# Kernel tuning notes

Measured on AMD Instinct MI355X. Metric: run time of the kernel, lower is better.

Reference implementation:

```python
import jax, jax.numpy as jnp
import numpy as np

EPS = 1e-6
NUM_HEADS = 16

def layernorm(x, alpha, bias):
    # Faithful to the torch module: torch.std uses ddof=1, and eps is added to std.
    mean = jnp.mean(x, axis=-1, keepdims=True)
    std = jnp.std(x, axis=-1, keepdims=True, ddof=1)
    return alpha * (x - mean) / (std + EPS) + bias

def setup_inputs() -> dict:
    key = jax.random.key(0)
    B, S, D, F = 4, 2048, 1024, 4096
    ks = jax.random.split(key, 8)
    s = 1.0 / np.sqrt(D)
    inp = {
        'x': jax.random.normal(ks[0], (B, S, D), jnp.float32),
        'src_mask': jnp.ones((B, 1, 1, S), jnp.int32),
        'wq': jax.random.normal(ks[1], (D, D), jnp.float32) * s,
        'bq': jnp.zeros((D,), jnp.float32),
        'wk': jax.random.normal(ks[2], (D, D), jnp.float32) * s,
        'bk': jnp.zeros((D,), jnp.float32),
        'wv': jax.random.normal(ks[3], (D, D), jnp.float32) * s,
        'bv': jnp.zeros((D,), jnp.float32),
        'wo': jax.random.normal(ks[4], (D, D), jnp.float32) * s,
        'bo': jnp.zeros((D,), jnp.float32),
        'w1': jax.random.normal(ks[5], (D, F), jnp.float32) * s,
        'b1': jnp.zeros((F,), jnp.float32),
        'w2': jax.random.normal(ks[6], (F, D), jnp.float32) * (1.0 / np.sqrt(F)),
        'b2': jnp.zeros((D,), jnp.float32),
        'ln1_a': jnp.ones((D,), jnp.float32),
        'ln1_b': jnp.zeros((D,), jnp.float32),
        'ln2_a': jnp.ones((D,), jnp.float32),
        'ln2_b': jnp.zeros((D,), jnp.float32),
    }
    return inp

def mha(x, src_mask, wq, bq, wk, bk, wv, bv, wo, bo):
    B, S, D = x.shape
    H = NUM_HEADS
    dk = D // H
    q = (x @ wq + bq).reshape(B, S, H, dk).transpose(0, 2, 1, 3)  # [B,H,S,dk]
    k = (x @ wk + bk).reshape(B, S, H, dk).transpose(0, 2, 1, 3)
    v = (x @ wv + bv).reshape(B, S, H, dk).transpose(0, 2, 1, 3)
    scores = jnp.einsum('bhqd,bhkd->bhqk', q, k) / np.sqrt(dk)  # [B,H,S,S]
    scores = jnp.where(src_mask == 0, -1e9, scores)
    p = jax.nn.softmax(scores, axis=-1)
    ctx = jnp.einsum('bhqk,bhkd->bhqd', p, v)  # [B,H,S,dk]
    ctx = ctx.transpose(0, 2, 1, 3).reshape(B, S, D)
    return ctx @ wo + bo

def reference(x, src_mask, wq, bq, wk, bk, wv, bv, wo, bo,
              w1, b1, w2, b2, ln1_a, ln1_b, ln2_a, ln2_b):
    # residual 1: pre-norm self-attention (dropout is identity in eval)
    h = x + mha(layernorm(x, ln1_a, ln1_b), src_mask, wq, bq, wk, bk, wv, bv, wo, bo)
    # residual 2: pre-norm FFN
    hn = layernorm(h, ln2_a, ln2_b)
    ffn = jax.nn.relu(hn @ w1 + b1) @ w2 + b2
    return h + ffn
```

## Files before the change

### kernel.cpp

```cpp
#include <hip/hip_runtime.h>
#include <hip/hip_bf16.h>

typedef __attribute__((ext_vector_type(8))) short bf16x8;
typedef __attribute__((ext_vector_type(4))) short bf16x4;
typedef __attribute__((ext_vector_type(4))) float f32x4;
typedef __hip_bfloat16 bf16;
typedef unsigned short u16;

#define B_ 4
#define S_ 2048
#define D_ 1024
#define F_ 4096
#define H_ 16
#define MROWS 8192
#define QSCALE 0.18033688011116012f

__device__ __forceinline__ unsigned pkbf(float lo, float hi){
  union{float f; unsigned u;} a, b; a.f = lo; b.f = hi;
  return __builtin_amdgcn_perm(b.u + 0x8000u, a.u + 0x8000u, 0x07060302);
}
__device__ __forceinline__ u16 bfrnd(float f){
  union{float ff; unsigned u;} c; c.ff = f;
  return (u16)((c.u + 0x8000u) >> 16);
}
__device__ __forceinline__ void gll16(const bf16* gp, u16* lp){
  __builtin_amdgcn_global_load_lds(
      (const __attribute__((address_space(1))) void*)gp,
      (__attribute__((address_space(3))) void*)lp, 16, 0, 0);
}

struct PrepArgs { const float* w[6]; const float* b[3]; };
__global__ __launch_bounds__(256) void prep(
    PrepArgs pa, bf16* __restrict__ wqkvoT, bf16* __restrict__ w1T,
    bf16* __restrict__ w2T, float* __restrict__ bqkv)
{
  __shared__ float tl[32][33];
  const int bid = blockIdx.x, tid = threadIdx.x;
  const int x = tid&31, y = tid>>5;
  if (bid < 12288) {
    const float* W; bf16* dst; int K, N, nb, kb;
    if (bid < 4096)      { int wi=bid>>10, t=bid&1023; W=pa.w[wi]; dst=wqkvoT+(size_t)wi*1048576; K=1024; N=1024; nb=t&31;  kb=t>>5; }
    else if (bid < 8192) { int t=bid-4096;             W=pa.w[4];  dst=w1T;  K=1024; N=4096; nb=t&127; kb=t>>7; }
    else                 { int t=bid-8192;             W=pa.w[5];  dst=w2T;  K=4096; N=1024; nb=t&31;  kb=t>>5; }
    const int n0=nb*32, k0=kb*32;
    #pragma unroll
    for (int i=0;i<32;i+=8)
      tl[y+i][x] = W[(size_t)(k0+y+i)*N + n0+x];
    __syncthreads();
    #pragma unroll
    for (int i=0;i<32;i+=8)
      dst[(size_t)(n0+y+i)*K + k0+x] = __float2bfloat16(tl[x][y+i]);
  } else {
    for (int i=tid; i<3072; i+=256) bqkv[i] = pa.b[i>>10][i&1023];
  }
}

__global__ __launch_bounds__(256) void v_transpose(
    const bf16* __restrict__ qkv, bf16* __restrict__ vT)
{
  __shared__ u16 tile[64*65];
  const int bh = blockIdx.y, b = bh>>4, h = bh&15;
  const int s0 = blockIdx.x*64;
  const int tid = threadIdx.x;
  const bf16* src = qkv + (size_t)(b*S_ + s0)*3072 + 2048 + h*64;
  #pragma unroll
  for (int i=0;i<2;i++){
    int idx = i*256 + tid;
    int r = idx>>3, sg = idx&7;
    uint4 v = *reinterpret_cast<const uint4*>(src + (size_t)r*3072 + sg*8);
    const u16* e = (const u16*)&v;
    #pragma unroll
    for (int j=0;j<8;j++) tile[r*65 + sg*8 + j] = e[j];
  }
  __syncthreads();
  bf16* dst = vT + (size_t)bh*64*S_ + s0;
  #pragma unroll
  for (int i=0;i<2;i++){
    int idx = i*256 + tid;
    int d = idx>>3, sg = idx&7;
    u16 tmp[8];
    #pragma unroll
    for (int j=0;j<8;j++) tmp[j] = tile[(sg*8+j)*65 + d];
    *reinterpret_cast<uint4*>(dst + (size_t)d*S_ + sg*8) = *reinterpret_cast<uint4*>(tmp);
  }
}

__device__ __forceinline__ float block_reduce_256(float v, float* sbuf){
  #pragma unroll
  for (int o=32;o>0;o>>=1) v += __shfl_down(v, o);
  int wave = threadIdx.x>>6;
  if ((threadIdx.x&63)==0) sbuf[wave] = v;
  __syncthreads();
  float r = sbuf[0]+sbuf[1]+sbuf[2]+sbuf[3];
  __syncthreads();
  return r;
}

__global__ __launch_bounds__(256) void ln_fwd(
    const float* __restrict__ x, const float* __restrict__ alpha,
    const float* __restrict__ beta, bf16* __restrict__ out)
{
  __shared__ float sbuf[4];
  int row = blockIdx.x, tid = threadIdx.x;
  const float4* xr = reinterpret_cast<const float4*>(x + (size_t)row*D_);
  float4 v = xr[tid];
  float sum = block_reduce_256(v.x+v.y+v.z+v.w, sbuf);
  float mean = sum * (1.0f/1024.0f);
  float dx0=v.x-mean, dx1=v.y-mean, dx2=v.z-mean, dx3=v.w-mean;
  float ssq = block_reduce_256(dx0*dx0+dx1*dx1+dx2*dx2+dx3*dx3, sbuf);
  float std_ = sqrtf(ssq * (1.0f/1023.0f));
  float inv = 1.0f/(std_ + 1e-6f);
  const float4* ar = reinterpret_cast<const float4*>(alpha);
  const float4* br = reinterpret_cast<const float4*>(beta);
  float4 a = ar[tid], bb = br[tid];
  unsigned* o = reinterpret_cast<unsigned*>(out + (size_t)row*D_);
  o[tid*2+0] = pkbf(a.x*dx0*inv + bb.x, a.y*dx1*inv + bb.y);
  o[tid*2+1] = pkbf(a.z*dx2*inv + bb.z, a.w*dx3*inv + bb.w);
}

template<int EPI>
__global__ __launch_bounds__(512) void gemm_bt(
    const bf16* __restrict__ A, const bf16* __restrict__ BT,
    const float* __restrict__ bias, const float* __restrict__ res,
    void* __restrict__ out, int M, int N, int K)
{
  __shared__ __align__(16) u16 As[128*32];
  __shared__ __align__(16) u16 Bs[128*32];
  const int tid = threadIdx.x;
  const int m0 = blockIdx.x*128, n0 = blockIdx.y*128;
  const int wave = tid>>6, lane = tid&63;
  const int wm = (wave>>2)*64, wn = (wave&3)*32;
  const int lrow = lane&15, quad = lane>>4;
  const int srow = wave*16 + (lane>>2);
  const int sseg = lane&3;
  const bf16* apg = A  + (size_t)(m0+srow)*K + sseg*8;
  const bf16* bpg = BT + (size_t)(n0+srow)*K + sseg*8;
  u16* asd = &As[wave*512];
  u16* bsd = &Bs[wave*512];

  f32x4 acc[4][2];
  #pragma unroll
  for (int i=0;i<4;i++)
    #pragma unroll
    for (int j=0;j<2;j++) acc[i][j] = (f32x4){0.f,0.f,0.f,0.f};

  for (int k0=0; k0<K; k0+=32) {
    gll16(apg + k0, asd);
    gll16(bpg + k0, bsd);
    __syncthreads();
    bf16x8 a[4], b[2];
    #pragma unroll
    for (int t=0;t<4;t++)
      a[t] = *reinterpret_cast<const bf16x8*>(&As[(wm + t*16 + lrow)*32 + quad*8]);
    #pragma unroll
    for (int t=0;t<2;t++)
      b[t] = *reinterpret_cast<const bf16x8*>(&Bs[(wn + t*16 + lrow)*32 + quad*8]);
    #pragma unroll
    for (int mt=0;mt<4;mt++)
      #pragma unroll
      for (int nt=0;nt<2;nt++)
        acc[mt][nt] = __builtin_amdgcn_mfma_f32_16x16x32_bf16(a[mt], b[nt], acc[mt][nt], 0,0,0);
    __syncthreads();
  }

  #pragma unroll
  for (int mt=0;mt<4;mt++){
    #pragma unroll
    for (int nt=0;nt<2;nt++){
      int col = n0 + wn + nt*16 + lrow;
      float bv = bias[col];
      float sc = (EPI == 3 && col < 1024) ? QSCALE : 1.0f;
      #pragma unroll
      for (int r=0;r<4;r++){
        int row = m0 + wm + mt*16 + quad*4 + r;
        size_t idx = (size_t)row*N + col;
        float val = acc[mt][nt][r] + bv;
        if (EPI == 1) val = fmaxf(val, 0.0f);
        if (EPI == 3) val *= sc;
        if (EPI == 2) {
          ((float*)out)[idx] = val + res[idx];
        } else {
          ((u16*)out)[idx] = bfrnd(val);
        }
      }
    }
  }
}

#define LA256(bu,hf) (lds + (((bu)*2+0)*2+(hf))*8192)
#define LB256(bu,hf) (lds + (((bu)*2+1)*2+(hf))*8192)

__device__ __forceinline__ bf16x8 ldfrag(const u16* base, int row, int chunk){
  int pc = chunk ^ (row & 7);
  return *reinterpret_cast<const bf16x8*>(base + row*64 + pc*8);
}

__device__ __forceinline__ void stage_half256(const bf16* __restrict__ src, int K,
                                              u16* lbase, int wave, int lane){
  #pragma unroll
  for (int i=0;i<2;i++){
    int q = i*512 + wave*64 + lane;
    int row = q>>3;
    int seg = (q&7) ^ (row&7);
    gll16(src + (size_t)row*K + seg*8, lbase + (i*512 + wave*64)*8);
  }
}

template<int RH, int KS, bool RB, typename STG, typename TAIL>
__device__ __forceinline__ void gphase(const u16* pa, const u16* pb, int bcol,
    int lr, int quad, bf16x8 (&b)[4][2], f32x4 (&acc)[8][4], STG stg, TAIL tail)
{
  bf16x8 a_[4];
  #pragma unroll
  for (int ar=0; ar<4; ar++)
    a_[ar] = ldfrag(pa, RH*64 + ar*16 + lr, KS*4 + quad);
  if constexpr (RB){
    #pragma unroll
    for (int cb=0; cb<4; cb++){
      b[cb][0] = ldfrag(pb, bcol + cb*16 + lr, quad);
      b[cb][1] = ldfrag(pb, bcol + cb*16 + lr, 4 + quad);
    }
  }
  stg();
  __builtin_amdgcn_s_barrier();
  asm volatile("s_waitcnt lgkmcnt(0)" ::: "memory");
  __builtin_amdgcn_sched_barrier(0);
  __builtin_amdgcn_s_setprio(1);
  #pragma unroll
  for (int ar=0; ar<4; ar++)
    #pragma unroll
    for (int cb=0; cb<4; cb++)
      acc[RH*4+ar][cb] = __builtin_amdgcn_mfma_f32_16x16x32_bf16(a_[ar], b[cb][KS], acc[RH*4+ar][cb], 0,0,0);
  __builtin_amdgcn_s_setprio(0);
  tail();
  __builtin_amdgcn_s_barrier();
}

template<int EPI>
__global__ __launch_bounds__(512) void gemm256(
    const bf16* __restrict__ A, const bf16* __restrict__ BT,
    const float* __restrict__ bias, bf16* __restrict__ out, int N, int K)
{
  __shared__ __align__(16) u16 lds[65536];
  const int tid = threadIdx.x, wave = tid>>6, lane = tid&63;
  const int wr = wave>>2, wc = wave&3;
  const int lr = lane&15, quad = lane>>4;
  const int gx = gridDim.x;
  const int nwg = gx*gridDim.y;
  int flat = blockIdx.y*gx + blockIdx.x;
  int cpx = nwg>>3;
  int swz = (flat&7)*cpx + (flat>>3);
  const int m0 = (swz % gx)*256, n0 = (swz / gx)*256;
  const int T = K>>6;

  const bf16* Ag = A  + (size_t)m0*K;
  const bf16* Bg = BT + (size_t)n0*K;
  const int bcol = (wc&1)*64;

  f32x4 acc[8][4];
  #pragma unroll
  for (int i=0;i<8;i++)
    #pragma unroll
    for (int j=0;j<4;j++) acc[i][j] = (f32x4){0.f,0.f,0.f,0.f};

  stage_half256(Ag,                       K, LA256(0,0), wave, lane);
  stage_half256(Ag + (size_t)128*K,       K, LA256(0,1), wave, lane);
  stage_half256(Bg,                       K, LB256(0,0), wave, lane);
  stage_half256(Bg + (size_t)128*K,       K, LB256(0,1), wave, lane);
  stage_half256(Bg + 64,                  K, LB256(1,0), wave, lane);
  stage_half256(Bg + (size_t)128*K + 64,  K, LB256(1,1), wave, lane);
  asm volatile("s_waitcnt vmcnt(4)" ::: "memory");
  __builtin_amdgcn_s_barrier();

  for (int t=0; t<T; ++t){
    const int bu = t&1, nbu = bu^1;
    const u16* pa = LA256(bu, wr);
    const u16* pb = LB256(bu, wc>>1);
    const size_t ktA = (size_t)((t+1 < T) ? t+1 : T-1)*64;
    const size_t ktB = (size_t)((t+2 < T) ? t+2 : T-1)*64;
    bf16x8 b[4][2];
    gphase<0,0,true >(pa, pb, bcol, lr, quad, b, acc,
        [&]{ stage_half256(Ag + ktA,                 K, LA256(nbu,0), wave, lane); }, [&]{});
    gphase<1,0,false>(pa, pb, bcol, lr, quad, b, acc,
        [&]{ stage_half256(Ag + (size_t)128*K + ktA, K, LA256(nbu,1), wave, lane); }, [&]{});
    gphase<0,1,false>(pa, pb, bcol, lr, quad, b, acc,
        [&]{ stage_half256(Bg + ktB,                 K, LB256(bu,0),  wave, lane); }, [&]{});
    gphase<1,1,false>(pa, pb, bcol, lr, quad, b, acc,
        [&]{ stage_half256(Bg + (size_t)128*K + ktB, K, LB256(bu,1),  wave, lane); },
        [&]{ asm volatile("s_waitcnt vmcnt(4)" ::: "memory"); });
  }

  #pragma unroll
  for (int mi=0; mi<8; mi++){
    const int row0 = m0 + wr*128 + (mi>>2)*64 + (mi&3)*16 + quad*4;
    #pragma unroll
    for (int cb=0; cb<4; cb++){
      const int col = n0 + wc*64 + cb*16 + lr;
      float bv = bias[col];
      float sc = (EPI==3 && col < 1024) ? QSCALE : 1.0f;
      #pragma unroll
      for (int r=0; r<4; r++){
        float val = acc[mi][cb][r] + bv;
        if (EPI == 1) val = fmaxf(val, 0.0f);
        if (EPI == 3) val *= sc;
        ((u16*)out)[(size_t)(row0+r)*N + col] = bfrnd(val);
      }
    }
  }
}

#define LA2(bu,hf) (lds2 + ((bu)*3+(hf))*8192)
#define LB2(bu)    (lds2 + ((bu)*3+2)*8192)

template<int RH, int KS, bool RB, typename STG, typename TAIL>
__device__ __forceinline__ void gphase2(const u16* pa, const u16* pb, int bcol,
    int lr, int quad, bf16x8 (&b)[2][2], f32x4 (&acc)[8][2], STG stg, TAIL tail)
{
  bf16x8 a_[4];
  #pragma unroll
  for (int ar=0; ar<4; ar++)
    a_[ar] = ldfrag(pa, RH*64 + ar*16 + lr, KS*4 + quad);
  if constexpr (RB){
    #pragma unroll
    for (int cb=0; cb<2; cb++){
      b[cb][0] = ldfrag(pb, bcol + cb*16 + lr, quad);
      b[cb][1] = ldfrag(pb, bcol + cb*16 + lr, 4 + quad);
    }
  }
  stg();
  __builtin_amdgcn_s_barrier();
  asm volatile("s_waitcnt lgkmcnt(0)" ::: "memory");
  __builtin_amdgcn_sched_barrier(0);
  __builtin_amdgcn_s_setprio(1);
  #pragma unroll
  for (int ar=0; ar<4; ar++)
    #pragma unroll
    for (int cb=0; cb<2; cb++)
      acc[RH*4+ar][cb] = __builtin_amdgcn_mfma_f32_16x16x32_bf16(a_[ar], b[cb][KS], acc[RH*4+ar][cb], 0,0,0);
  __builtin_amdgcn_s_setprio(0);
  tail();
  __builtin_amdgcn_s_barrier();
}

__global__ __launch_bounds__(512) void gemm256r(
    const bf16* __restrict__ A, const bf16* __restrict__ BT,
    const float* __restrict__ bias, const float* __restrict__ res,
    float* __restrict__ out, int N, int K)
{
  __shared__ __align__(16) u16 lds2[49152];
  const int tid = threadIdx.x, wave = tid>>6, lane = tid&63;
  const int wr = wave>>2, wc = wave&3;
  const int lr = lane&15, quad = lane>>4;
  const int gx = gridDim.x;
  const int nwg = gx*gridDim.y;
  int flat = blockIdx.y*gx + blockIdx.x;
  int cpx = nwg>>3;
  int swz = (flat&7)*cpx + (flat>>3);
  const int m0 = (swz % gx)*256, n0 = (swz / gx)*128;
  const int T = K>>6;

  const bf16* Ag = A  + (size_t)m0*K;
  const bf16* Bg = BT + (size_t)n0*K;
  const int bcol = wc*32;

  f32x4 acc[8][2];
  #pragma unroll
  for (int i=0;i<8;i++)
    #pragma unroll
    for (int j=0;j<2;j++) acc[i][j] = (f32x4){0.f,0.f,0.f,0.f};

  stage_half256(Ag,                 K, LA2(0,0), wave, lane);
  stage_half256(Ag + (size_t)128*K, K, LA2(0,1), wave, lane);
  stage_half256(Bg,                 K, LB2(0),   wave, lane);
  stage_half256(Bg + 64,            K, LB2(1),   wave, lane);
  asm volatile("s_waitcnt vmcnt(2)" ::: "memory");
  __builtin_amdgcn_s_barrier();

  for (int t=0; t<T; ++t){
    const int bu = t&1, nbu = bu^1;
    const u16* pa = LA2(bu, wr);
    const u16* pb = LB2(bu);
    const size_t ktA = (size_t)((t+1 < T) ? t+1 : T-1)*64;
    const size_t ktB = (size_t)((t+2 < T) ? t+2 : T-1)*64;
    bf16x8 b[2][2];
    gphase2<0,0,true >(pa, pb, bcol, lr, quad, b, acc,
        [&]{ stage_half256(Ag + ktA,                 K, LA2(nbu,0), wave, lane); }, [&]{});
    gphase2<1,0,false>(pa, pb, bcol, lr, quad, b, acc,
        [&]{ stage_half256(Ag + (size_t)128*K + ktA, K, LA2(nbu,1), wave, lane); }, [&]{});
    gphase2<0,1,false>(pa, pb, bcol, lr, quad, b, acc,
        [&]{ stage_half256(Bg + ktB,                 K, LB2(bu),    wave, lane); }, [&]{});
    gphase2<1,1,false>(pa, pb, bcol, lr, quad, b, acc,
        [&]{}, [&]{ asm volatile("s_waitcnt vmcnt(2)" ::: "memory"); });
  }

  #pragma unroll
  for (int mi=0; mi<8; mi++){
    const int row0 = m0 + wr*128 + (mi>>2)*64 + (mi&3)*16 + quad*4;
    #pragma unroll
    for (int cb=0; cb<2; cb++){
      const int col = n0 + bcol + cb*16 + lr;
      float bv = bias[col];
      #pragma unroll
      for (int r=0; r<4; r++){
        size_t idx = (size_t)(row0+r)*N + col;
        out[idx] = acc[mi][cb][r] + bv + res[idx];
      }
    }
  }
}

#define KP 72

__global__ __launch_bounds__(512) void flash_attn_mfma(
    const bf16* __restrict__ qkv, const bf16* __restrict__ vT,
    const int* __restrict__ mask, bf16* __restrict__ ctx)
{
  __shared__ __align__(16) u16 Ks[64*KP];
  __shared__ __align__(16) u16 Vt[64*KP];
  __shared__ __align__(16) float Mb[64];

  const int b = blockIdx.z, h = blockIdx.y, qt = blockIdx.x;
  const int tid = threadIdx.x, wave = tid>>6, lane = tid&63;
  const int lr = lane&15, quad = lane>>4;
  const int qbase = qt*256 + wave*32;

  const bf16* base = qkv + (size_t)b*S_*3072 + h*64;
  const bf16* vtb  = vT + (size_t)(b*H_+h)*64*S_;
  const int*  mrow = mask + b*S_;

  bf16x8 qf[2][2];
  #pragma unroll
  for (int c=0;c<2;c++){
    const bf16* qp = base + (size_t)(qbase + c*16 + lr)*3072 + quad*8;
    qf[c][0] = *reinterpret_cast<const bf16x8*>(qp);
    qf[c][1] = *reinterpret_cast<const bf16x8*>(qp + 32);
  }

  const bf16x4 ones4 = {(short)0x3F80,(short)0x3F80,(short)0x3F80,(short)0x3F80};

  f32x4 actx[2][4];
  f32x4 acc_l[2];
  #pragma unroll
  for (int c=0;c<2;c++){
    #pragma unroll
    for (int dt=0;dt<4;dt++) actx[c][dt] = (f32x4){0.f,0.f,0.f,0.f};
    acc_l[c] = (f32x4){0.f,0.f,0.f,0.f};
  }

  const int sr = tid>>3, sg = tid&7;

  for (int kt=0; kt<S_; kt+=64){
    *reinterpret_cast<uint4*>(&Ks[sr*KP + sg*8]) =
      *reinterpret_cast<const uint4*>(base + 1024 + (size_t)(kt+sr)*3072 + sg*8);
    *reinterpret_cast<uint4*>(&Vt[sr*KP + sg*8]) =
      *reinterpret_cast<const uint4*>(vtb + (size_t)sr*S_ + kt + sg*8);
    if (tid < 64) Mb[tid] = (mrow[kt+tid]==0) ? -2e9f : 0.0f;
    unsigned long long bal = __ballot(mrow[kt + lane] == 0);
    __syncthreads();

    bf16x4 pk[2][4];
    if (bal == 0ULL) {
      #pragma unroll
      for (int nt=0;nt<4;nt++){
        bf16x8 kf0 = *reinterpret_cast<const bf16x8*>(&Ks[(nt*16+lr)*KP + quad*8]);
        bf16x8 kf1 = *reinterpret_cast<const bf16x8*>(&Ks[(nt*16+lr)*KP + 32 + quad*8]);
        #pragma unroll
        for (int c=0;c<2;c++){
          f32x4 a = (f32x4){0.f,0.f,0.f,0.f};
          a = __builtin_amdgcn_mfma_f32_16x16x32_bf16(kf0, qf[c][0], a, 0,0,0);
          a = __builtin_amdgcn_mfma_f32_16x16x32_bf16(kf1, qf[c][1], a, 0,0,0);
          uint2 w;
          w.x = pkbf(__builtin_amdgcn_exp2f(a[0]), __builtin_amdgcn_exp2f(a[1]));
          w.y = pkbf(__builtin_amdgcn_exp2f(a[2]), __builtin_amdgcn_exp2f(a[3]));
          union{uint2 u; bf16x4 v;} cvt; cvt.u = w;
          pk[c][nt] = cvt.v;
        }
      }
    } else {
      #pragma unroll
      for (int nt=0;nt<4;nt++){
        bf16x8 kf0 = *reinterpret_cast<const bf16x8*>(&Ks[(nt*16+lr)*KP + quad*8]);
        bf16x8 kf1 = *reinterpret_cast<const bf16x8*>(&Ks[(nt*16+lr)*KP + 32 + quad*8]);
        float4 mb = *reinterpret_cast<const float4*>(&Mb[nt*16 + quad*4]);
        #pragma unroll
        for (int c=0;c<2;c++){
          f32x4 a = (f32x4){0.f,0.f,0.f,0.f};
          a = __builtin_amdgcn_mfma_f32_16x16x32_bf16(kf0, qf[c][0], a, 0,0,0);
          a = __builtin_amdgcn_mfma_f32_16x16x32_bf16(kf1, qf[c][1], a, 0,0,0);
          uint2 w;
          w.x = pkbf(__builtin_amdgcn_exp2f(a[0]+mb.x), __builtin_amdgcn_exp2f(a[1]+mb.y));
          w.y = pkbf(__builtin_amdgcn_exp2f(a[2]+mb.z), __builtin_amdgcn_exp2f(a[3]+mb.w));
          union{uint2 u; bf16x4 v;} cvt; cvt.u = w;
          pk[c][nt] = cvt.v;
        }
      }
    }

    #pragma unroll
    for (int dt=0;dt<4;dt++){
      #pragma unroll
      for (int kc=0;kc<4;kc++){
        bf16x4 vf = *reinterpret_cast<const bf16x4*>(&Vt[(dt*16+lr)*KP + kc*16 + quad*4]);
        #pragma unroll
        for (int c=0;c<2;c++)
          actx[c][dt] = __builtin_amdgcn_mfma_f32_16x16x16bf16_1k(vf, pk[c][kc], actx[c][dt], 0,0,0);
      }
    }
    #pragma unroll
    for (int kc=0;kc<4;kc++)
      #pragma unroll
      for (int c=0;c<2;c++)
        acc_l[c] = __builtin_amdgcn_mfma_f32_16x16x16bf16_1k(ones4, pk[c][kc], acc_l[c], 0,0,0);
    __syncthreads();
  }

  #pragma unroll
  for (int c=0;c<2;c++){
    float inv = 1.0f/acc_l[c][0];
    int q = qbase + c*16 + lr;
    bf16* op = ctx + (size_t)(b*S_+q)*D_ + h*64 + quad*4;
    #pragma unroll
    for (int dt=0;dt<4;dt++){
      uint2 o;
      o.x = pkbf(actx[c][dt][0]*inv, actx[c][dt][1]*inv);
      o.y = pkbf(actx[c][dt][2]*inv, actx[c][dt][3]*inv);
      *reinterpret_cast<uint2*>(op + dt*16) = o;
    }
  }
}

extern "C" void kernel_launch(void* const* d_in, const int* in_sizes, int n_in,
                              void* d_out, int out_size, void* d_ws, size_t ws_size,
                              hipStream_t stream) {
  const float* x    = (const float*)d_in[0];
  const int*   mask = (const int*)  d_in[1];
  const float* wq   = (const float*)d_in[2];
  const float* bq   = (const float*)d_in[3];
  const float* wk   = (const float*)d_in[4];
  const float* bk   = (const float*)d_in[5];
  const float* wv   = (const float*)d_in[6];
  const float* bv   = (const float*)d_in[7];
  const float* wo   = (const float*)d_in[8];
  const float* bo   = (const float*)d_in[9];
  const float* w1   = (const float*)d_in[10];
  const float* b1   = (const float*)d_in[11];
  const float* w2   = (const float*)d_in[12];
  const float* b2   = (const float*)d_in[13];
  const float* ln1a = (const float*)d_in[14];
  const float* ln1b = (const float*)d_in[15];
  const float* ln2a = (const float*)d_in[16];
  const float* ln2b = (const float*)d_in[17];

  char* ws = (char*)d_ws;
  bf16*  wqkvT = (bf16*) (ws + 0);
  bf16*  woT   = (bf16*) (ws + 6291456);
  bf16*  w1T   = (bf16*) (ws + 8388608);
  bf16*  w2T   = (bf16*) (ws + 16777216);
  float* bqkv  = (float*)(ws + 25165824);
  bf16*  xn    = (bf16*) (ws + 25178112);
  bf16*  vT    = (bf16*) (ws + 25178112);
  bf16*  qkv   = (bf16*) (ws + 41955328);
  bf16*  ctx   = (bf16*) (ws + 92286976);
  bf16*  hn    = (bf16*) (ws + 109064192);
  bf16*  act   = (bf16*) (ws + 25178112);

  PrepArgs pa;
  pa.w[0]=wq; pa.w[1]=wk; pa.w[2]=wv; pa.w[3]=wo; pa.w[4]=w1; pa.w[5]=w2;
  pa.b[0]=bq; pa.b[1]=bk; pa.b[2]=bv;
  prep<<<12289,256,0,stream>>>(pa, wqkvT, w1T, w2T, bqkv);

  ln_fwd<<<8192,256,0,stream>>>(x, ln1a, ln1b, xn);
  gemm256<3><<<dim3(32,12),512,0,stream>>>(xn, wqkvT, bqkv, qkv, 3072, 1024);
  v_transpose<<<dim3(32,64),256,0,stream>>>(qkv, vT);
  flash_attn_mfma<<<dim3(S_/256,H_,B_),512,0,stream>>>(qkv, vT, mask, ctx);
  gemm256r<<<dim3(32,8),512,0,stream>>>(ctx, woT, bo, x, (float*)d_out, 1024, 1024);
  ln_fwd<<<8192,256,0,stream>>>((const float*)d_out, ln2a, ln2b, hn);
  gemm256<1><<<dim3(32,16),512,0,stream>>>(hn, w1T, b1, act, F_, 1024);
  gemm256r<<<dim3(32,8),512,0,stream>>>(act, w2T, b2, (const float*)d_out, (float*)d_out, 1024, 4096);
}
```

Measured before the change: 526.4 us.

## Rework flash attention to 32x32x16 MFMA with VALU row-sum and lane shuffles

Rebuilds the attention inner loop around 32x32x16 bf16 MFMA tiles for both QK^T and PV, instead of 16x16 tiles. Each wave now covers 32 query rows with a single accumulator layout. The softmax denominator is accumulated on the VALU from the rounded bf16 probabilities, replacing the extra ones-vector MFMAs. Cross-half lane shuffles rearrange the P fragments into the B-operand layout. It also adds an occupancy hint to the launch bounds, which may increase register pressure or spilling.

```diff
diff --git a/kernel.cpp b/kernel.cpp
--- a/kernel.cpp
+++ b/kernel.cpp
@@ -4,6 +4,7 @@
 typedef __attribute__((ext_vector_type(8))) short bf16x8;
 typedef __attribute__((ext_vector_type(4))) short bf16x4;
 typedef __attribute__((ext_vector_type(4))) float f32x4;
+typedef __attribute__((ext_vector_type(16))) float f32x16;
 typedef __hip_bfloat16 bf16;
 typedef unsigned short u16;
 
@@ -411,7 +412,7 @@
 
 #define KP 72
 
-__global__ __launch_bounds__(512) void flash_attn_mfma(
+__global__ __launch_bounds__(512,4) void flash_attn_mfma(
     const bf16* __restrict__ qkv, const bf16* __restrict__ vT,
     const int* __restrict__ mask, bf16* __restrict__ ctx)
 {
@@ -419,33 +420,29 @@
   __shared__ __align__(16) u16 Vt[64*KP];
   __shared__ __align__(16) float Mb[64];
 
-  const int b = blockIdx.z, h = blockIdx.y, qt = blockIdx.x;
+  const int b = blockIdx.z, head = blockIdx.y, qt = blockIdx.x;
   const int tid = threadIdx.x, wave = tid>>6, lane = tid&63;
-  const int lr = lane&15, quad = lane>>4;
+  const int lq = lane&31, hv = lane>>5;
   const int qbase = qt*256 + wave*32;
 
-  const bf16* base = qkv + (size_t)b*S_*3072 + h*64;
-  const bf16* vtb  = vT + (size_t)(b*H_+h)*64*S_;
+  const bf16* base = qkv + (size_t)b*S_*3072 + head*64;
+  const bf16* vtb  = vT + (size_t)(b*H_+head)*64*S_;
   const int*  mrow = mask + b*S_;
 
-  bf16x8 qf[2][2];
-  #pragma unroll
-  for (int c=0;c<2;c++){
-    const bf16* qp = base + (size_t)(qbase + c*16 + lr)*3072 + quad*8;
-    qf[c][0] = *reinterpret_cast<const bf16x8*>(qp);
-    qf[c][1] = *reinterpret_cast<const bf16x8*>(qp + 32);
-  }
-
-  const bf16x4 ones4 = {(short)0x3F80,(short)0x3F80,(short)0x3F80,(short)0x3F80};
-
-  f32x4 actx[2][4];
-  f32x4 acc_l[2];
-  #pragma unroll
-  for (int c=0;c<2;c++){
-    #pragma unroll
-    for (int dt=0;dt<4;dt++) actx[c][dt] = (f32x4){0.f,0.f,0.f,0.f};
-    acc_l[c] = (f32x4){0.f,0.f,0.f,0.f};
-  }
+  bf16x8 qf[4];
+  {
+    const bf16* qp = base + (size_t)(qbase + lq)*3072 + hv*8;
+    #pragma unroll
+    for (int i=0;i<4;i++)
+      qf[i] = *reinterpret_cast<const bf16x8*>(qp + i*16);
+  }
+
+  f32x16 actx[2];
+  #pragma unroll
+  for (int dt=0;dt<2;dt++)
+    #pragma unroll
+    for (int i=0;i<16;i++) actx[dt][i] = 0.f;
+  float l_run = 0.f;
 
   const int sr = tid>>3, sg = tid&7;
 
@@ -458,73 +455,79 @@
     unsigned long long bal = __ballot(mrow[kt + lane] == 0);
     __syncthreads();
 
-    bf16x4 pk[2][4];
-    if (bal == 0ULL) {
-      #pragma unroll
-      for (int nt=0;nt<4;nt++){
-        bf16x8 kf0 = *reinterpret_cast<const bf16x8*>(&Ks[(nt*16+lr)*KP + quad*8]);
-        bf16x8 kf1 = *reinterpret_cast<const bf16x8*>(&Ks[(nt*16+lr)*KP + 32 + quad*8]);
+    #pragma unroll
+    for (int ks=0; ks<2; ks++){
+      f32x16 s;
+      #pragma unroll
+      for (int i=0;i<16;i++) s[i] = 0.f;
+      #pragma unroll
+      for (int i=0;i<4;i++){
+        bf16x8 kf = *reinterpret_cast<const bf16x8*>(&Ks[(ks*32+lq)*KP + i*16 + hv*8]);
+        s = __builtin_amdgcn_mfma_f32_32x32x16_bf16(kf, qf[i], s, 0,0,0);
+      }
+      uint2 ch[4];
+      #pragma unroll
+      for (int g=0; g<4; g++){
+        float e0,e1,e2,e3;
+        if (bal == 0ULL){
+          e0 = __builtin_amdgcn_exp2f(s[4*g+0]);
+          e1 = __builtin_amdgcn_exp2f(s[4*g+1]);
+          e2 = __builtin_amdgcn_exp2f(s[4*g+2]);
+          e3 = __builtin_amdgcn_exp2f(s[4*g+3]);
+        } else {
+          float4 mb = *reinterpret_cast<const float4*>(&Mb[ks*32 + g*8 + hv*4]);
+          e0 = __builtin_amdgcn_exp2f(s[4*g+0] + mb.x);
+          e1 = __builtin_amdgcn_exp2f(s[4*g+1] + mb.y);
+          e2 = __builtin_amdgcn_exp2f(s[4*g+2] + mb.z);
+          e3 = __builtin_amdgcn_exp2f(s[4*g+3] + mb.w);
+        }
+        union{float f; unsigned u;} c0,c1,c2,c3;
+        c0.f = e0; c1.f = e1; c2.f = e2; c3.f = e3;
+        unsigned u0 = c0.u + 0x8000u, u1 = c1.u + 0x8000u;
+        unsigned u2 = c2.u + 0x8000u, u3 = c3.u + 0x8000u;
+        union{unsigned u; float f;} r0,r1,r2,r3;
+        r0.u = u0 & 0xffff0000u; r1.u = u1 & 0xffff0000u;
+        r2.u = u2 & 0xffff0000u; r3.u = u3 & 0xffff0000u;
+        l_run += (r0.f + r1.f) + (r2.f + r3.f);
+        ch[g].x = __builtin_amdgcn_perm(u1, u0, 0x07060302);
+        ch[g].y = __builtin_amdgcn_perm(u3, u2, 0x07060302);
+      }
+      uint2 sw[4];
+      #pragma unroll
+      for (int g=0; g<4; g++){
+        sw[g].x = __shfl_xor((int)ch[g].x, 32);
+        sw[g].y = __shfl_xor((int)ch[g].y, 32);
+      }
+      #pragma unroll
+      for (int m=0; m<2; m++){
+        union{unsigned u[4]; bf16x8 v;} fb;
+        fb.u[0] = hv ? sw[2*m+1].x : ch[2*m].x;
+        fb.u[1] = hv ? sw[2*m+1].y : ch[2*m].y;
+        fb.u[2] = hv ? ch[2*m+1].x : sw[2*m].x;
+        fb.u[3] = hv ? ch[2*m+1].y : sw[2*m].y;
         #pragma unroll
-        for (int c=0;c<2;c++){
-          f32x4 a = (f32x4){0.f,0.f,0.f,0.f};
-          a = __builtin_amdgcn_mfma_f32_16x16x32_bf16(kf0, qf[c][0], a, 0,0,0);
-          a = __builtin_amdgcn_mfma_f32_16x16x32_bf16(kf1, qf[c][1], a, 0,0,0);
-          uint2 w;
-          w.x = pkbf(__builtin_amdgcn_exp2f(a[0]), __builtin_amdgcn_exp2f(a[1]));
-          w.y = pkbf(__builtin_amdgcn_exp2f(a[2]), __builtin_amdgcn_exp2f(a[3]));
-          union{uint2 u; bf16x4 v;} cvt; cvt.u = w;
-          pk[c][nt] = cvt.v;
+        for (int dt=0; dt<2; dt++){
+          bf16x8 vf = *reinterpret_cast<const bf16x8*>(
+              &Vt[(dt*32+lq)*KP + ks*32 + m*16 + hv*8]);
+          actx[dt] = __builtin_amdgcn_mfma_f32_32x32x16_bf16(vf, fb.v, actx[dt], 0,0,0);
         }
       }
-    } else {
-      #pragma unroll
-      for (int nt=0;nt<4;nt++){
-        bf16x8 kf0 = *reinterpret_cast<const bf16x8*>(&Ks[(nt*16+lr)*KP + quad*8]);
-        bf16x8 kf1 = *reinterpret_cast<const bf16x8*>(&Ks[(nt*16+lr)*KP + 32 + quad*8]);
-        float4 mb = *reinterpret_cast<const float4*>(&Mb[nt*16 + quad*4]);
-        #pragma unroll
-        for (int c=0;c<2;c++){
-          f32x4 a = (f32x4){0.f,0.f,0.f,0.f};
-          a = __builtin_amdgcn_mfma_f32_16x16x32_bf16(kf0, qf[c][0], a, 0,0,0);
-          a = __builtin_amdgcn_mfma_f32_16x16x32_bf16(kf1, qf[c][1], a, 0,0,0);
-          uint2 w;
-          w.x = pkbf(__builtin_amdgcn_exp2f(a[0]+mb.x), __builtin_amdgcn_exp2f(a[1]+mb.y));
-          w.y = pkbf(__builtin_amdgcn_exp2f(a[2]+mb.z), __builtin_amdgcn_exp2f(a[3]+mb.w));
-          union{uint2 u; bf16x4 v;} cvt; cvt.u = w;
-          pk[c][nt] = cvt.v;
-        }
-      }
-    }
-
-    #pragma unroll
-    for (int dt=0;dt<4;dt++){
-      #pragma unroll
-      for (int kc=0;kc<4;kc++){
-        bf16x4 vf = *reinterpret_cast<const bf16x4*>(&Vt[(dt*16+lr)*KP + kc*16 + quad*4]);
-        #pragma unroll
-        for (int c=0;c<2;c++)
-          actx[c][dt] = __builtin_amdgcn_mfma_f32_16x16x16bf16_1k(vf, pk[c][kc], actx[c][dt], 0,0,0);
-      }
-    }
-    #pragma unroll
-    for (int kc=0;kc<4;kc++)
-      #pragma unroll
-      for (int c=0;c<2;c++)
-        acc_l[c] = __builtin_amdgcn_mfma_f32_16x16x16bf16_1k(ones4, pk[c][kc], acc_l[c], 0,0,0);
+    }
     __syncthreads();
   }
 
-  #pragma unroll
-  for (int c=0;c<2;c++){
-    float inv = 1.0f/acc_l[c][0];
-    int q = qbase + c*16 + lr;
-    bf16* op = ctx + (size_t)(b*S_+q)*D_ + h*64 + quad*4;
-    #pragma unroll
-    for (int dt=0;dt<4;dt++){
+  float lfull = l_run + __shfl_xor(l_run, 32);
+  float inv = 1.0f/lfull;
+  int q = qbase + lq;
+  bf16* op = ctx + (size_t)(b*S_+q)*D_ + head*64;
+  #pragma unroll
+  for (int dt=0; dt<2; dt++){
+    #pragma unroll
+    for (int g=0; g<4; g++){
       uint2 o;
-      o.x = pkbf(actx[c][dt][0]*inv, actx[c][dt][1]*inv);
-      o.y = pkbf(actx[c][dt][2]*inv, actx[c][dt][3]*inv);
-      *reinterpret_cast<uint2*>(op + dt*16) = o;
+      o.x = pkbf(actx[dt][4*g+0]*inv, actx[dt][4*g+1]*inv);
+      o.y = pkbf(actx[dt][4*g+2]*inv, actx[dt][4*g+3]*inv);
+      *reinterpret_cast<uint2*>(op + dt*32 + g*8 + hv*4) = o;
     }
   }
 }
```

Result: no change. 529.7 us (+0.6%).

## Double-buffer K/V tiles in flash attention with register prefetch

Applied to the files above, without the earlier changes.

The flash attention loop now prefetches the next K, V and mask tile into registers before computing on the current tile, then stores them into a second LDS buffer after the MFMA work, so each iteration needs one barrier instead of two. This is meant to hide global load latency behind the score and PV computation. In exchange it doubles LDS use and raises register pressure, which could lower occupancy at 512 threads per block.

```diff
diff --git a/kernel.cpp b/kernel.cpp
--- a/kernel.cpp
+++ b/kernel.cpp
@@ -415,9 +415,9 @@
     const bf16* __restrict__ qkv, const bf16* __restrict__ vT,
     const int* __restrict__ mask, bf16* __restrict__ ctx)
 {
-  __shared__ __align__(16) u16 Ks[64*KP];
-  __shared__ __align__(16) u16 Vt[64*KP];
-  __shared__ __align__(16) float Mb[64];
+  __shared__ __align__(16) u16 Ks[2][64*KP];
+  __shared__ __align__(16) u16 Vt[2][64*KP];
+  __shared__ __align__(16) float Mb[2][64];
 
   const int b = blockIdx.z, h = blockIdx.y, qt = blockIdx.x;
   const int tid = threadIdx.x, wave = tid>>6, lane = tid&63;
@@ -448,22 +448,36 @@
   }
 
   const int sr = tid>>3, sg = tid&7;
-
-  for (int kt=0; kt<S_; kt+=64){
-    *reinterpret_cast<uint4*>(&Ks[sr*KP + sg*8]) =
-      *reinterpret_cast<const uint4*>(base + 1024 + (size_t)(kt+sr)*3072 + sg*8);
-    *reinterpret_cast<uint4*>(&Vt[sr*KP + sg*8]) =
-      *reinterpret_cast<const uint4*>(vtb + (size_t)sr*S_ + kt + sg*8);
-    if (tid < 64) Mb[tid] = (mrow[kt+tid]==0) ? -2e9f : 0.0f;
-    unsigned long long bal = __ballot(mrow[kt + lane] == 0);
-    __syncthreads();
+  const bf16* kgp = base + 1024 + (size_t)sr*3072 + sg*8;
+  const bf16* vgp = vtb + (size_t)sr*S_ + sg*8;
+
+  {
+    uint4 k0 = *reinterpret_cast<const uint4*>(kgp);
+    uint4 v0 = *reinterpret_cast<const uint4*>(vgp);
+    *reinterpret_cast<uint4*>(&Ks[0][sr*KP + sg*8]) = k0;
+    *reinterpret_cast<uint4*>(&Vt[0][sr*KP + sg*8]) = v0;
+  }
+  int mcur = mrow[lane];
+  if (tid < 64) Mb[0][tid] = (mcur==0) ? -2e9f : 0.0f;
+  __syncthreads();
+
+  int ti = 0;
+  for (int kt=0; kt<S_; kt+=64, ti^=1){
+    const bool more = (kt+64 < S_);
+    uint4 kreg, vreg; int mnext = 1;
+    if (more){
+      kreg = *reinterpret_cast<const uint4*>(kgp + (size_t)(kt+64)*3072);
+      vreg = *reinterpret_cast<const uint4*>(vgp + kt + 64);
+      mnext = mrow[kt + 64 + lane];
+    }
+    unsigned long long bal = __ballot(mcur == 0);
 
     bf16x4 pk[2][4];
     if (bal == 0ULL) {
       #pragma unroll
       for (int nt=0;nt<4;nt++){
-        bf16x8 kf0 = *reinterpret_cast<const bf16x8*>(&Ks[(nt*16+lr)*KP + quad*8]);
-        bf16x8 kf1 = *reinterpret_cast<const bf16x8*>(&Ks[(nt*16+lr)*KP + 32 + quad*8]);
+        bf16x8 kf0 = *reinterpret_cast<const bf16x8*>(&Ks[ti][(nt*16+lr)*KP + quad*8]);
+        bf16x8 kf1 = *reinterpret_cast<const bf16x8*>(&Ks[ti][(nt*16+lr)*KP + 32 + quad*8]);
         #pragma unroll
         for (int c=0;c<2;c++){
           f32x4 a = (f32x4){0.f,0.f,0.f,0.f};
@@ -479,9 +493,9 @@
     } else {
       #pragma unroll
       for (int nt=0;nt<4;nt++){
-        bf16x8 kf0 = *reinterpret_cast<const bf16x8*>(&Ks[(nt*16+lr)*KP + quad*8]);
-        bf16x8 kf1 = *reinterpret_cast<const bf16x8*>(&Ks[(nt*16+lr)*KP + 32 + quad*8]);
-        float4 mb = *reinterpret_cast<const float4*>(&Mb[nt*16 + quad*4]);
+        bf16x8 kf0 = *reinterpret_cast<const bf16x8*>(&Ks[ti][(nt*16+lr)*KP + quad*8]);
+        bf16x8 kf1 = *reinterpret_cast<const bf16x8*>(&Ks[ti][(nt*16+lr)*KP + 32 + quad*8]);
+        float4 mb = *reinterpret_cast<const float4*>(&Mb[ti][nt*16 + quad*4]);
         #pragma unroll
         for (int c=0;c<2;c++){
           f32x4 a = (f32x4){0.f,0.f,0.f,0.f};
@@ -500,7 +514,7 @@
     for (int dt=0;dt<4;dt++){
       #pragma unroll
       for (int kc=0;kc<4;kc++){
-        bf16x4 vf = *reinterpret_cast<const bf16x4*>(&Vt[(dt*16+lr)*KP + kc*16 + quad*4]);
+        bf16x4 vf = *reinterpret_cast<const bf16x4*>(&Vt[ti][(dt*16+lr)*KP + kc*16 + quad*4]);
         #pragma unroll
         for (int c=0;c<2;c++)
           actx[c][dt] = __builtin_amdgcn_mfma_f32_16x16x16bf16_1k(vf, pk[c][kc], actx[c][dt], 0,0,0);
@@ -511,6 +525,13 @@
       #pragma unroll
       for (int c=0;c<2;c++)
         acc_l[c] = __builtin_amdgcn_mfma_f32_16x16x16bf16_1k(ones4, pk[c][kc], acc_l[c], 0,0,0);
+
+    if (more){
+      *reinterpret_cast<uint4*>(&Ks[ti^1][sr*KP + sg*8]) = kreg;
+      *reinterpret_cast<uint4*>(&Vt[ti^1][sr*KP + sg*8]) = vreg;
+      if (tid < 64) Mb[ti^1][tid] = (mnext==0) ? -2e9f : 0.0f;
+    }
+    mcur = mnext;
     __syncthreads();
   }
 
```

Measured after the change: 524.7 us. No clear change (-0.3%).
